# Kernel optimization log

Measured on AMD Instinct MI355X. Metric: run time of the kernel, lower is better.

## Reference

```python
import jax, jax.numpy as jnp
import numpy as np

L, D, FF, V, B, S, H, GS = 6, 1024, 4096, 32000, 2, 1024, 16, 128
DH = D // H


def setup_inputs() -> dict:
    key = jax.random.key(0)
    ks = jax.random.split(key, 32)

    def tern(k, shape):
        # ternary values in {-1, 0, 1}, stored as float32 (int8 buffer in torch)
        return jax.random.randint(k, shape, -1, 2).astype(jnp.float32)

    def sc(k, shape):
        # positive per-group scales (abs-mean init, clamped > 0)
        return jax.random.uniform(k, shape, jnp.float32, 0.01, 0.1)

    inp = {
        'input_ids': jax.random.randint(ks[0], (B, S), 0, V),
        'emb_t': tern(ks[1], (V, D)),
        'emb_s': sc(ks[2], (V * D // GS,)),
        'pos_emb': jax.random.normal(ks[3], (S, D), jnp.float32) * 0.02,
        'q_t': tern(ks[4], (L, D, D)), 'q_s': sc(ks[5], (L, D * D // GS)),
        'k_t': tern(ks[6], (L, D, D)), 'k_s': sc(ks[7], (L, D * D // GS)),
        'v_t': tern(ks[8], (L, D, D)), 'v_s': sc(ks[9], (L, D * D // GS)),
        'o_t': tern(ks[10], (L, D, D)), 'o_s': sc(ks[11], (L, D * D // GS)),
        'g_t': tern(ks[12], (L, FF, D)), 'g_s': sc(ks[13], (L, D * FF // GS)),
        'u_t': tern(ks[14], (L, FF, D)), 'u_s': sc(ks[15], (L, D * FF // GS)),
        'd_t': tern(ks[16], (L, D, FF)), 'd_s': sc(ks[17], (L, D * FF // GS)),
        'alpha': jnp.full((L, H, 1, 1), 0.1, jnp.float32),
        'na_w': jnp.ones((L, D), jnp.float32),
        'nm_w': jnp.ones((L, D), jnp.float32),
        'nf_w': jnp.ones((D,), jnp.float32),
        'head_t': tern(ks[18], (V, D)),
        'head_s': sc(ks[19], (V * D // GS,)),
    }
    return inp


def _dq(t, s):
    # dequantize: reshape ternary to (..., n_groups, GS), scale per group
    tg = t.reshape(t.shape[:-2] + (-1, GS))
    return (tg * s[..., :, None]).reshape(t.shape)


def _rms(x, w, eps=1e-6):
    return x * jax.lax.rsqrt(jnp.mean(x * x, axis=-1, keepdims=True) + eps) * w


def _forward(input_ids, emb_t, emb_s, pos_emb, q_t, q_s, k_t, k_s, v_t, v_s,
             o_t, o_s, g_t, g_s, u_t, u_s, d_t, d_s, alpha, na_w, nm_w, nf_w,
             head_t, head_s):
    x = _dq(emb_t, emb_s)[input_ids] + pos_emb[None, :S]  # [B,S,D]
    causal = jnp.tril(jnp.ones((S, S), bool))
    scale = DH ** -0.5

    def block(x, p):
        (qt, qs, kt, ks_, vt, vs, ot, os_, gt, gs_, ut, us, dt, ds,
         al, naw, nmw) = p
        h = _rms(x, naw)

        def proj(t, s):
            return (h @ _dq(t, s).T).reshape(B, S, H, DH).transpose(0, 2, 1, 3)

        q, k, v = proj(qt, qs), proj(kt, ks_), proj(vt, vs)
        att = jnp.einsum('bhqd,bhkd->bhqk', q, k) * scale
        att = jax.nn.softmax(jnp.where(causal, att, -jnp.inf), axis=-1)
        out = jnp.einsum('bhqk,bhkd->bhqd', att, v)
        # residual head-mix: out += alpha * x_heads (x here is the normed input h)
        out = out + al * h.reshape(B, S, H, DH).transpose(0, 2, 1, 3)
        out = out.transpose(0, 2, 1, 3).reshape(B, S, D)
        x = x + out @ _dq(ot, os_).T
        h2 = _rms(x, nmw)
        gate = h2 @ _dq(gt, gs_).T
        up = h2 @ _dq(ut, us).T
        x = x + (jax.nn.silu(gate) * up) @ _dq(dt, ds).T
        return x, None

    params = (q_t, q_s, k_t, k_s, v_t, v_s, o_t, o_s, g_t, g_s, u_t, u_s,
              d_t, d_s, alpha, na_w, nm_w)
    x, _ = jax.lax.scan(block, x, params)
    x = _rms(x, nf_w)
    return x @ _dq(head_t, head_s).T  # [B,S,V]


def reference(input_ids, emb_t, emb_s, pos_emb, q_t, q_s, k_t, k_s, v_t, v_s,
              o_t, o_s, g_t, g_s, u_t, u_s, d_t, d_s, alpha, na_w, nm_w, nf_w,
              head_t, head_s):
    return _forward(input_ids, emb_t, emb_s, pos_emb, q_t, q_s, k_t, k_s,
                    v_t, v_s, o_t, o_s, g_t, g_s, u_t, u_s, d_t, d_s,
                    alpha, na_w, nm_w, nf_w, head_t, head_s)
```

## Files before the change

### kernel.cpp

```cpp
#include <hip/hip_runtime.h>
#include <math.h>

#define Lc   6
#define Dc   1024
#define FFc  4096
#define Vc   32000
#define Bc   2
#define Sc   1024
#define Hc   16
#define GSc  128
#define DHc  64
#define Mc   (Bc * Sc)

typedef __attribute__((ext_vector_type(8))) short bf16x8;
typedef __attribute__((ext_vector_type(4))) float f32x4;

__device__ inline unsigned ph2(float a, float b) {
    return (__float_as_uint(b) & 0xffff0000u) | (__float_as_uint(a) >> 16);
}
__device__ inline float flo(float a) {
    return a - __uint_as_float(__float_as_uint(a) & 0xffff0000u);
}
__device__ inline ushort bhi(float a) { return (ushort)(__float_as_uint(a) >> 16); }
__device__ inline ushort blo(float a) { return (ushort)(__float_as_uint(flo(a)) >> 16); }
__device__ inline float unbf(ushort h) { return __uint_as_float((unsigned)h << 16); }

__device__ inline size_t swz_bidx(int row, int col, int K) {
    size_t byte = (size_t)col * 2;
    size_t base = (size_t)row * K * 2 + (byte & ~(size_t)127);
    int inner = (int)(byte & 127);
    inner = (inner & 15) | ((((inner >> 4) ^ (row & 7)) & 7) << 4);
    return base + (size_t)inner;
}

__device__ inline void glds16(const void* g, void* l) {
    __builtin_amdgcn_global_load_lds(
        (const __attribute__((address_space(1))) void*)g,
        (__attribute__((address_space(3))) void*)l, 16, 0, 0);
}

__device__ inline float block_reduce_sum(float v, float* scratch) {
    __syncthreads();
    int lane = threadIdx.x & 63, w = threadIdx.x >> 6;
#pragma unroll
    for (int off = 32; off > 0; off >>= 1) v += __shfl_down(v, off, 64);
    if (lane == 0) scratch[w] = v;
    __syncthreads();
    if (threadIdx.x == 0) scratch[0] = scratch[0] + scratch[1] + scratch[2] + scratch[3];
    __syncthreads();
    return scratch[0];
}

__global__ __launch_bounds__(256) void k_embed(const int* __restrict__ ids,
                                               const float* __restrict__ et,
                                               const float* __restrict__ es,
                                               const float* __restrict__ pos,
                                               float* __restrict__ x) {
    int row = blockIdx.x;
    int sp  = row & (Sc - 1);
    int d   = threadIdx.x << 2;
    int idx = ids[row];
    int base = idx * Dc + d;
    float4 t = *(const float4*)(et + base);
    float  s = es[base >> 7];
    float4 p = *(const float4*)(pos + sp * Dc + d);
    float4 o;
    o.x = fmaf(t.x, s, p.x); o.y = fmaf(t.y, s, p.y);
    o.z = fmaf(t.z, s, p.z); o.w = fmaf(t.w, s, p.w);
    *(float4*)(x + row * Dc + d) = o;
}

__global__ __launch_bounds__(256) void k_rmsnorm_bf(const float* __restrict__ x,
                                                    const float* __restrict__ w,
                                                    ushort* __restrict__ hi,
                                                    ushort* __restrict__ lo) {
    __shared__ float scratch[4];
    int row = blockIdx.x;
    int d = threadIdx.x << 2;
    float4 f = *(const float4*)(x + (size_t)row * Dc + d);
    float s = f.x * f.x + f.y * f.y + f.z * f.z + f.w * f.w;
    s = block_reduce_sum(s, scratch);
    float rinv = rsqrtf(s * (1.0f / Dc) + 1e-6f);
    float4 wv = *(const float4*)(w + d);
    float o0 = f.x * rinv * wv.x, o1 = f.y * rinv * wv.y;
    float o2 = f.z * rinv * wv.z, o3 = f.w * rinv * wv.w;
    ushort4 hv, lv;
    hv.x = bhi(o0); hv.y = bhi(o1); hv.z = bhi(o2); hv.w = bhi(o3);
    lv.x = blo(o0); lv.y = blo(o1); lv.z = blo(o2); lv.w = blo(o3);
    const size_t sb = swz_bidx(row, d, Dc);
    *(ushort4*)((char*)hi + sb) = hv;
    *(ushort4*)((char*)lo + sb) = lv;
}

template <bool RESID>
__device__ __forceinline__ void gemm_core(
    const ushort* __restrict__ Ahi, const ushort* __restrict__ Alo,
    const float* __restrict__ Wt, const float* __restrict__ Ws,
    const float* __restrict__ R, float* __restrict__ C,
    const int bn, const int N, const int K, const int g0, const int g1) {
    __shared__ char Ah[16384];
    __shared__ char Al[16384];
    __shared__ char Bh[16384];
    __shared__ float Wsl[128];

    const int tid  = threadIdx.x;
    const int lane = tid & 63;
    const int wv   = tid >> 6;
    const int wm   = (wv >> 1) << 6;
    const int wn   = (wv & 1) << 6;
    const int bm   = blockIdx.x << 7;
    const int kg   = K >> 7;

    const int sr   = tid >> 1;
    const int sh   = tid & 1;
    const int swr  = (sr & 7) << 4;
    const int rowb = sr << 7;
    const int colb = sh << 6;
    const float* Bbase = Wt + (size_t)(bn + sr) * K + (sh << 5);

    const int gr = (wv << 3) + (lane >> 3);
    const int gc = (lane & 7) << 4;
    const char* Abh = (const char*)Ahi;
    const char* Abl = (const char*)Alo;

    const int lr  = lane & 15;
    const int lkb = (lane >> 4) << 4;
    const int frs = (lane & 7) << 4;

    f32x4 acc[4][4], accg[4][4];
#pragma unroll
    for (int i = 0; i < 4; ++i)
#pragma unroll
        for (int j = 0; j < 4; ++j) {
            acc[i][j]  = (f32x4){0.f, 0.f, 0.f, 0.f};
            accg[i][j] = (f32x4){0.f, 0.f, 0.f, 0.f};
        }

    float4 bv[8];
    const int s0 = g0 << 1, s1 = g1 << 1;
    {
        const float4* p = (const float4*)(Bbase + (s0 << 6));
#pragma unroll
        for (int jj = 0; jj < 8; ++jj) bv[jj] = p[jj];
    }

    for (int s = s0; s < s1; ++s) {
        const int k0 = s << 6;
        __syncthreads();
#pragma unroll
        for (int i = 0; i < 4; ++i) {
            const size_t sb = ((size_t)(bm + gr + (i << 5)) * K + k0) * 2 + gc;
            glds16(Abh + sb, Ah + (wv << 10) + (i << 12));
            glds16(Abl + sb, Al + (wv << 10) + (i << 12));
        }
        if ((s & 1) == 0 && tid < 128)
            Wsl[tid] = Ws[(size_t)(bn + tid) * kg + (s >> 1)];
#pragma unroll
        for (int j = 0; j < 4; ++j) {
            const int ob = rowb + ((colb + (j << 4)) ^ swr);
            float4 x0 = bv[2 * j], x1 = bv[2 * j + 1];
            *(uint4*)(Bh + ob) = make_uint4(ph2(x0.x, x0.y), ph2(x0.z, x0.w),
                                            ph2(x1.x, x1.y), ph2(x1.z, x1.w));
        }
        __syncthreads();
        if (s + 1 < s1) {
            const float4* p = (const float4*)(Bbase + ((s + 1) << 6));
#pragma unroll
            for (int jj = 0; jj < 8; ++jj) bv[jj] = p[jj];
        }
#pragma unroll
        for (int ks = 0; ks < 2; ++ks) {
            bf16x8 fa[4], fl[4], fb[4];
            const int cb = ((ks << 6) + lkb) ^ frs;
#pragma unroll
            for (int f = 0; f < 4; ++f) {
                const int ra = (wm + (f << 4) + lr) << 7;
                fa[f] = *(const bf16x8*)(Ah + ra + cb);
                fl[f] = *(const bf16x8*)(Al + ra + cb);
                const int rb = (wn + (f << 4) + lr) << 7;
                fb[f] = *(const bf16x8*)(Bh + rb + cb);
            }
#pragma unroll
            for (int i = 0; i < 4; ++i)
#pragma unroll
                for (int j = 0; j < 4; ++j) {
                    accg[i][j] = __builtin_amdgcn_mfma_f32_16x16x32_bf16(fa[i], fb[j], accg[i][j], 0, 0, 0);
                    accg[i][j] = __builtin_amdgcn_mfma_f32_16x16x32_bf16(fl[i], fb[j], accg[i][j], 0, 0, 0);
                }
        }
        if (s & 1) {
            float sv[4];
#pragma unroll
            for (int j = 0; j < 4; ++j) sv[j] = Wsl[wn + (j << 4) + lr];
#pragma unroll
            for (int i = 0; i < 4; ++i)
#pragma unroll
                for (int j = 0; j < 4; ++j) {
                    acc[i][j] += accg[i][j] * sv[j];
                    accg[i][j] = (f32x4){0.f, 0.f, 0.f, 0.f};
                }
        }
    }

    const int r0 = bm + wm + ((lane >> 4) << 2);
    const int c0 = bn + wn + lr;
#pragma unroll
    for (int i = 0; i < 4; ++i) {
        const int row = r0 + (i << 4);
#pragma unroll
        for (int j = 0; j < 4; ++j) {
            size_t off = (size_t)row * N + c0 + (j << 4);
#pragma unroll
            for (int e = 0; e < 4; ++e) {
                float vv = acc[i][j][e];
                if (RESID) vv += R[off];
                C[off] = vv;
                off += (size_t)N;
            }
        }
    }
}

template <bool RESID>
__global__ __launch_bounds__(256, 2) void k_gemm_bfa(
    const ushort* __restrict__ Ahi, const ushort* __restrict__ Alo,
    const float* __restrict__ Wt, const float* __restrict__ Ws,
    const float* __restrict__ R, float* __restrict__ C, int N, int K) {
    gemm_core<RESID>(Ahi, Alo, Wt, Ws, R, C, blockIdx.y << 7, N, K, 0, K >> 7);
}

__global__ __launch_bounds__(256, 2) void k_gemm_part(
    const ushort* __restrict__ Ahi, const ushort* __restrict__ Alo,
    const float* __restrict__ Wt, const float* __restrict__ Ws,
    float* __restrict__ P, int N, int K, int gper) {
    const int z = blockIdx.z;
    gemm_core<false>(Ahi, Alo, Wt, Ws, nullptr, P + (size_t)z * Mc * Dc,
                     blockIdx.y << 7, N, K, z * gper, (z + 1) * gper);
}

__global__ __launch_bounds__(256, 2) void k_gemm_qkv(
    const ushort* __restrict__ Ahi, const ushort* __restrict__ Alo,
    const float* __restrict__ qt, const float* __restrict__ qs,
    const float* __restrict__ kt, const float* __restrict__ ks,
    const float* __restrict__ vt, const float* __restrict__ vs,
    float* __restrict__ qb, float* __restrict__ kb, float* __restrict__ vb) {
    const int which = blockIdx.y >> 3;
    const int bn = (blockIdx.y & 7) << 7;
    const float* Wt = which == 0 ? qt : which == 1 ? kt : vt;
    const float* Ws = which == 0 ? qs : which == 1 ? ks : vs;
    float* C = which == 0 ? qb : which == 1 ? kb : vb;
    gemm_core<false>(Ahi, Alo, Wt, Ws, nullptr, C, bn, Dc, Dc, 0, Dc >> 7);
}

__global__ __launch_bounds__(256, 2) void k_gemm_gu(
    const ushort* __restrict__ Ahi, const ushort* __restrict__ Alo,
    const float* __restrict__ gt, const float* __restrict__ gs,
    const float* __restrict__ ut, const float* __restrict__ us,
    float* __restrict__ gate, float* __restrict__ up) {
    const int which = blockIdx.y >> 5;
    const int bn = (blockIdx.y & 31) << 7;
    const float* Wt = which == 0 ? gt : ut;
    const float* Ws = which == 0 ? gs : us;
    float* C = which == 0 ? gate : up;
    gemm_core<false>(Ahi, Alo, Wt, Ws, nullptr, C, bn, FFc, Dc, 0, Dc >> 7);
}

__global__ __launch_bounds__(256) void k_red4(const float* __restrict__ p,
                                              float* __restrict__ x) {
    const size_t i = (((size_t)blockIdx.x << 8) + threadIdx.x) << 2;
    const size_t st = (size_t)Mc * Dc;
    float4 a  = *(const float4*)(x + i);
    float4 p0 = *(const float4*)(p + i);
    float4 p1 = *(const float4*)(p + i + st);
    float4 p2 = *(const float4*)(p + i + 2 * st);
    float4 p3 = *(const float4*)(p + i + 3 * st);
    a.x += p0.x + p1.x + p2.x + p3.x;
    a.y += p0.y + p1.y + p2.y + p3.y;
    a.z += p0.z + p1.z + p2.z + p3.z;
    a.w += p0.w + p1.w + p2.w + p3.w;
    *(float4*)(x + i) = a;
}

__global__ __launch_bounds__(256) void k_silumul(const float* __restrict__ g,
                                                 const float* __restrict__ u,
                                                 ushort* __restrict__ fhi,
                                                 ushort* __restrict__ fl2) {
    const size_t i = (((size_t)blockIdx.x << 8) + threadIdx.x) << 2;
    float4 gv = *(const float4*)(g + i);
    float4 uv = *(const float4*)(u + i);
    float r0 = uv.x * (gv.x / (1.0f + expf(-gv.x)));
    float r1 = uv.y * (gv.y / (1.0f + expf(-gv.y)));
    float r2 = uv.z * (gv.z / (1.0f + expf(-gv.z)));
    float r3 = uv.w * (gv.w / (1.0f + expf(-gv.w)));
    ushort4 hv, lv;
    hv.x = bhi(r0); hv.y = bhi(r1); hv.z = bhi(r2); hv.w = bhi(r3);
    lv.x = blo(r0); lv.y = blo(r1); lv.z = blo(r2); lv.w = blo(r3);
    const int row = (int)(i >> 12);
    const int col = (int)(i & 4095);
    const size_t sb = swz_bidx(row, col, FFc);
    *(ushort4*)((char*)fhi + sb) = hv;
    *(ushort4*)((char*)fl2 + sb) = lv;
}

__global__ __launch_bounds__(256, 2) void k_attn_mfma(
    const float* __restrict__ q, const float* __restrict__ k,
    const float* __restrict__ v, const ushort* __restrict__ hnhi,
    const ushort* __restrict__ hnlo, const float* __restrict__ alpha,
    ushort* __restrict__ aohi, ushort* __restrict__ aolo) {
    __shared__ uint4 KhV[512], KlV[512];
    __shared__ uint4 VthV[512], VtlV[512];
    __shared__ uint4 PhV[512], PlV[512];
    char* Khc  = (char*)KhV;
    char* Klc  = (char*)KlV;
    char* Vthc = (char*)VthV;
    char* Vtlc = (char*)VtlV;

    const int t = blockIdx.x, hh = blockIdx.y, b = blockIdx.z;
    const int tid  = threadIdx.x;
    const int lane = tid & 63, w = tid >> 6;
    const int lr = lane & 15, g = lane >> 4;
    const int bS = b * Sc;
    const int hoff = hh * DHc;

    char* myPh = (char*)PhV + (w << 11);
    char* myPl = (char*)PlV + (w << 11);

    const int qrow = (t << 6) + (w << 4) + lr;
    bf16x8 qh[2], ql[2];
    {
        const float* qp = q + (size_t)(bS + qrow) * Dc + hoff + (g << 3);
#pragma unroll
        for (int c = 0; c < 2; ++c) {
            float4 f0 = *(const float4*)(qp + (c << 5));
            float4 f1 = *(const float4*)(qp + (c << 5) + 4);
            float s[8] = {f0.x * 0.125f, f0.y * 0.125f, f0.z * 0.125f, f0.w * 0.125f,
                          f1.x * 0.125f, f1.y * 0.125f, f1.z * 0.125f, f1.w * 0.125f};
            union { bf16x8 v; unsigned u[4]; } Hh, Ll;
#pragma unroll
            for (int p = 0; p < 4; ++p) {
                Hh.u[p] = ph2(s[2 * p], s[2 * p + 1]);
                Ll.u[p] = ph2(flo(s[2 * p]), flo(s[2 * p + 1]));
            }
            qh[c] = Hh.v; ql[c] = Ll.v;
        }
    }

    f32x4 oacc[4];
    float m[4], lsum[4];
#pragma unroll
    for (int f = 0; f < 4; ++f) oacc[f] = (f32x4){0.f, 0.f, 0.f, 0.f};
#pragma unroll
    for (int e = 0; e < 4; ++e) { m[e] = -3.0e38f; lsum[e] = 0.f; }

    const int skey = tid >> 2, sseg = tid & 3;
    const int k4 = (tid >> 4) << 2, d4 = (tid & 15) << 2;

    float4 kr[4], vr[4];
    {
        const float* src = k + (size_t)(bS + skey) * Dc + hoff + (sseg << 4);
#pragma unroll
        for (int r = 0; r < 4; ++r) kr[r] = *(const float4*)(src + (r << 2));
        const float* vsrc = v + (size_t)(bS + k4) * Dc + hoff + d4;
#pragma unroll
        for (int r = 0; r < 4; ++r) vr[r] = *(const float4*)(vsrc + r * Dc);
    }

    const int nt = t + 1;
    for (int j = 0; j < nt; ++j) {
        {
            const int swz = (skey & 7) << 4;
            char* dsth = Khc + skey * 128;
            char* dstl = Klc + skey * 128;
            float4 a0 = kr[0], a1 = kr[1], a2 = kr[2], a3 = kr[3];
            *(uint4*)(dsth + (((sseg << 5)) ^ swz)) =
                make_uint4(ph2(a0.x, a0.y), ph2(a0.z, a0.w), ph2(a1.x, a1.y), ph2(a1.z, a1.w));
            *(uint4*)(dsth + (((sseg << 5) + 16) ^ swz)) =
                make_uint4(ph2(a2.x, a2.y), ph2(a2.z, a2.w), ph2(a3.x, a3.y), ph2(a3.z, a3.w));
            *(uint4*)(dstl + (((sseg << 5)) ^ swz)) =
                make_uint4(ph2(flo(a0.x), flo(a0.y)), ph2(flo(a0.z), flo(a0.w)),
                           ph2(flo(a1.x), flo(a1.y)), ph2(flo(a1.z), flo(a1.w)));
            *(uint4*)(dstl + (((sseg << 5) + 16) ^ swz)) =
                make_uint4(ph2(flo(a2.x), flo(a2.y)), ph2(flo(a2.z), flo(a2.w)),
                           ph2(flo(a3.x), flo(a3.y)), ph2(flo(a3.z), flo(a3.w)));
        }
        {
            union { float4 v4; float f[4]; } r0, r1, r2, r3;
            r0.v4 = vr[0]; r1.v4 = vr[1]; r2.v4 = vr[2]; r3.v4 = vr[3];
#pragma unroll
            for (int d = 0; d < 4; ++d) {
                const int dh = d4 + d;
                const int byt = dh * 128 + (((k4 << 1)) ^ ((dh & 7) << 4));
                float x0 = r0.f[d], x1 = r1.f[d], x2 = r2.f[d], x3 = r3.f[d];
                *(uint2*)(Vthc + byt) = make_uint2(ph2(x0, x1), ph2(x2, x3));
                *(uint2*)(Vtlc + byt) =
                    make_uint2(ph2(flo(x0), flo(x1)), ph2(flo(x2), flo(x3)));
            }
        }
        __syncthreads();
        if (j + 1 < nt) {
            const int kb2 = (j + 1) << 6;
            const float* src = k + (size_t)(bS + kb2 + skey) * Dc + hoff + (sseg << 4);
#pragma unroll
            for (int r = 0; r < 4; ++r) kr[r] = *(const float4*)(src + (r << 2));
            const float* vsrc = v + (size_t)(bS + kb2 + k4) * Dc + hoff + d4;
#pragma unroll
            for (int r = 0; r < 4; ++r) vr[r] = *(const float4*)(vsrc + r * Dc);
        }

        f32x4 sacc[4];
#pragma unroll
        for (int f = 0; f < 4; ++f) sacc[f] = (f32x4){0.f, 0.f, 0.f, 0.f};
#pragma unroll
        for (int c = 0; c < 2; ++c) {
            const int cb = (c << 6) + (g << 4);
#pragma unroll
            for (int f = 0; f < 4; ++f) {
                const int row = (f << 4) + lr;
                const int byt = row * 128 + (cb ^ ((row & 7) << 4));
                bf16x8 kh = *(const bf16x8*)(Khc + byt);
                bf16x8 kl = *(const bf16x8*)(Klc + byt);
                sacc[f] = __builtin_amdgcn_mfma_f32_16x16x32_bf16(qh[c], kh, sacc[f], 0, 0, 0);
                sacc[f] = __builtin_amdgcn_mfma_f32_16x16x32_bf16(ql[c], kh, sacc[f], 0, 0, 0);
                sacc[f] = __builtin_amdgcn_mfma_f32_16x16x32_bf16(qh[c], kl, sacc[f], 0, 0, 0);
            }
        }
        if (j == t) {
            const int qloc = (w << 4) + (g << 2);
#pragma unroll
            for (int f = 0; f < 4; ++f) {
                const int key = (f << 4) + lr;
#pragma unroll
                for (int e = 0; e < 4; ++e)
                    if (key > qloc + e) sacc[f][e] = -3.0e38f;
            }
        }
        float rmax[4], corr[4], rsum[4];
#pragma unroll
        for (int e = 0; e < 4; ++e)
            rmax[e] = fmaxf(fmaxf(sacc[0][e], sacc[1][e]), fmaxf(sacc[2][e], sacc[3][e]));
#pragma unroll
        for (int msk = 1; msk <= 8; msk <<= 1)
#pragma unroll
            for (int e = 0; e < 4; ++e)
                rmax[e] = fmaxf(rmax[e], __shfl_xor(rmax[e], msk, 64));
#pragma unroll
        for (int e = 0; e < 4; ++e) {
            float mn = fmaxf(m[e], rmax[e]);
            corr[e] = __expf(m[e] - mn);
            m[e] = mn;
            rsum[e] = 0.f;
        }
#pragma unroll
        for (int f = 0; f < 4; ++f)
#pragma unroll
            for (int e = 0; e < 4; ++e) {
                float p = __expf(sacc[f][e] - m[e]);
                sacc[f][e] = p;
                rsum[e] += p;
            }
#pragma unroll
        for (int msk = 1; msk <= 8; msk <<= 1)
#pragma unroll
            for (int e = 0; e < 4; ++e) rsum[e] += __shfl_xor(rsum[e], msk, 64);
#pragma unroll
        for (int e = 0; e < 4; ++e) lsum[e] = lsum[e] * corr[e] + rsum[e];
#pragma unroll
        for (int f = 0; f < 4; ++f)
#pragma unroll
            for (int e = 0; e < 4; ++e) oacc[f][e] *= corr[e];

#pragma unroll
        for (int f = 0; f < 4; ++f) {
            const int key2 = ((f << 4) + lr) << 1;
#pragma unroll
            for (int e = 0; e < 4; ++e) {
                const int qr = (g << 2) + e;
                const int byt = qr * 128 + (key2 ^ ((qr & 7) << 4));
                unsigned bits = __float_as_uint(sacc[f][e]);
                unsigned hib = bits & 0xffff0000u;
                *(short*)(myPh + byt) = (short)(hib >> 16);
                float lov = sacc[f][e] - __uint_as_float(hib);
                *(short*)(myPl + byt) = (short)(__float_as_uint(lov) >> 16);
            }
        }
#pragma unroll
        for (int c = 0; c < 2; ++c) {
            const int cb = (c << 6) + (g << 4);
            const int pbyt = lr * 128 + (cb ^ ((lr & 7) << 4));
            bf16x8 pah = *(const bf16x8*)(myPh + pbyt);
            bf16x8 pal = *(const bf16x8*)(myPl + pbyt);
#pragma unroll
            for (int f = 0; f < 4; ++f) {
                const int row = (f << 4) + lr;
                const int byt = row * 128 + (cb ^ ((row & 7) << 4));
                bf16x8 vbh = *(const bf16x8*)(Vthc + byt);
                bf16x8 vbl = *(const bf16x8*)(Vtlc + byt);
                oacc[f] = __builtin_amdgcn_mfma_f32_16x16x32_bf16(pah, vbh, oacc[f], 0, 0, 0);
                oacc[f] = __builtin_amdgcn_mfma_f32_16x16x32_bf16(pal, vbh, oacc[f], 0, 0, 0);
                oacc[f] = __builtin_amdgcn_mfma_f32_16x16x32_bf16(pah, vbl, oacc[f], 0, 0, 0);
            }
        }
        __syncthreads();
    }

    const float al = alpha[hh];
    float invl[4];
#pragma unroll
    for (int e = 0; e < 4; ++e) invl[e] = 1.0f / lsum[e];
#pragma unroll
    for (int f = 0; f < 4; ++f) {
        const int dh = (f << 4) + lr;
#pragma unroll
        for (int e = 0; e < 4; ++e) {
            const int qg = (t << 6) + (w << 4) + (g << 2) + e;
            const int row = bS + qg;
            const size_t sb = swz_bidx(row, hoff + dh, Dc);
            float hnv = unbf(*(const ushort*)((const char*)hnhi + sb)) +
                        unbf(*(const ushort*)((const char*)hnlo + sb));
            float val = fmaf(al, hnv, oacc[f][e] * invl[e]);
            *(ushort*)((char*)aohi + sb) = bhi(val);
            *(ushort*)((char*)aolo + sb) = blo(val);
        }
    }
}

extern "C" void kernel_launch(void* const* d_in, const int* in_sizes, int n_in,
                              void* d_out, int out_size, void* d_ws, size_t ws_size,
                              hipStream_t stream) {
    const int*   ids    = (const int*)d_in[0];
    const float* emb_t  = (const float*)d_in[1];
    const float* emb_s  = (const float*)d_in[2];
    const float* pos    = (const float*)d_in[3];
    const float* q_t    = (const float*)d_in[4];
    const float* q_s    = (const float*)d_in[5];
    const float* k_t    = (const float*)d_in[6];
    const float* k_s    = (const float*)d_in[7];
    const float* v_t    = (const float*)d_in[8];
    const float* v_s    = (const float*)d_in[9];
    const float* o_t    = (const float*)d_in[10];
    const float* o_s    = (const float*)d_in[11];
    const float* g_t    = (const float*)d_in[12];
    const float* g_s    = (const float*)d_in[13];
    const float* u_t    = (const float*)d_in[14];
    const float* u_s    = (const float*)d_in[15];
    const float* dd_t   = (const float*)d_in[16];
    const float* dd_s   = (const float*)d_in[17];
    const float* alpha  = (const float*)d_in[18];
    const float* na_w   = (const float*)d_in[19];
    const float* nm_w   = (const float*)d_in[20];
    const float* nf_w   = (const float*)d_in[21];
    const float* head_t = (const float*)d_in[22];
    const float* head_s = (const float*)d_in[23];
    float* outp = (float*)d_out;

    float*  ws   = (float*)d_ws;
    float*  x    = ws;
    ushort* hhi  = (ushort*)(x + (size_t)Mc * Dc);
    ushort* hlo  = hhi + (size_t)Mc * Dc;
    float*  big  = (float*)(hlo + (size_t)Mc * Dc);
    float*  qb   = big;
    float*  kb   = big + (size_t)Mc * Dc;
    float*  vb   = big + (size_t)2 * Mc * Dc;
    ushort* aohi = (ushort*)(big + (size_t)3 * Mc * Dc);
    ushort* aolo = aohi + (size_t)Mc * Dc;
    float*  up   = big;
    float*  gate = (float*)d_out;
    ushort* ffhi = (ushort*)((char*)d_out + (size_t)Mc * FFc * 4);
    ushort* fflo = ffhi + (size_t)Mc * FFc;

    k_embed<<<Mc, 256, 0, stream>>>(ids, emb_t, emb_s, pos, x);

    const dim3 gD(Mc / 128, Dc / 128);
    const dim3 gQKV(Mc / 128, 3 * Dc / 128);
    const dim3 gGU(Mc / 128, 2 * FFc / 128);
    const dim3 gDN(Mc / 128, Dc / 128, 4);
    const dim3 gH(Mc / 128, Vc / 128);
    const dim3 gA(Sc / 64, Hc, Bc);
    const int  gSilu = (Mc * FFc) / (256 * 4);
    const int  gRed  = (Mc * Dc) / (256 * 4);

    for (int l = 0; l < Lc; ++l) {
        const float* qt = q_t + (size_t)l * Dc * Dc;
        const float* qs = q_s + (size_t)l * (Dc * Dc / GSc);
        const float* kt = k_t + (size_t)l * Dc * Dc;
        const float* ks = k_s + (size_t)l * (Dc * Dc / GSc);
        const float* vt = v_t + (size_t)l * Dc * Dc;
        const float* vs = v_s + (size_t)l * (Dc * Dc / GSc);
        const float* ot = o_t + (size_t)l * Dc * Dc;
        const float* os = o_s + (size_t)l * (Dc * Dc / GSc);
        const float* gt = g_t + (size_t)l * FFc * Dc;
        const float* gs = g_s + (size_t)l * (FFc * Dc / GSc);
        const float* ut = u_t + (size_t)l * FFc * Dc;
        const float* us = u_s + (size_t)l * (FFc * Dc / GSc);
        const float* dt = dd_t + (size_t)l * Dc * FFc;
        const float* ds = dd_s + (size_t)l * (Dc * FFc / GSc);

        k_rmsnorm_bf<<<Mc, 256, 0, stream>>>(x, na_w + l * Dc, hhi, hlo);
        k_gemm_qkv<<<gQKV, 256, 0, stream>>>(hhi, hlo, qt, qs, kt, ks, vt, vs, qb, kb, vb);
        k_attn_mfma<<<gA, 256, 0, stream>>>(qb, kb, vb, hhi, hlo, alpha + l * Hc, aohi, aolo);
        k_gemm_bfa<true><<<gD, 256, 0, stream>>>(aohi, aolo, ot, os, x, x, Dc, Dc);
        k_rmsnorm_bf<<<Mc, 256, 0, stream>>>(x, nm_w + l * Dc, hhi, hlo);
        k_gemm_gu<<<gGU, 256, 0, stream>>>(hhi, hlo, gt, gs, ut, us, gate, up);
        k_silumul<<<gSilu, 256, 0, stream>>>(gate, up, ffhi, fflo);
        k_gemm_part<<<gDN, 256, 0, stream>>>(ffhi, fflo, dt, ds, big, Dc, FFc, 8);
        k_red4<<<gRed, 256, 0, stream>>>(big, x);
    }

    k_rmsnorm_bf<<<Mc, 256, 0, stream>>>(x, nf_w, hhi, hlo);
    k_gemm_bfa<false><<<gH, 256, 0, stream>>>(hhi, hlo, head_t, head_s, nullptr, outp, Vc, Dc);
}
```

Baseline: 3.144 ms.

## Pair causal attention tiles per block, split-K the O projection, raise GEMM occupancy

The attention kernel now gives each block two query tiles, t and its mirror from the end, so every block does the same amount of causal work and the grid is halved. The output projection moves from a residual-fused GEMM to a 4-way split-K partial GEMM followed by a reduction kernel, which adds more blocks for a small N=1024 GEMM. Launch bounds on the GEMM kernels go from 2 to 3 waves per SIMD, which may cause register spills. The split-K path adds an extra reduction pass and writes the partial sums through d_out as scratch.

```diff
diff --git a/kernel.cpp b/kernel.cpp
--- a/kernel.cpp
+++ b/kernel.cpp
@@ -38,6 +38,7 @@
         (const __attribute__((address_space(1))) void*)g,
         (__attribute__((address_space(3))) void*)l, 16, 0, 0);
 }
+
 
 __device__ inline float block_reduce_sum(float v, float* scratch) {
     __syncthreads();
@@ -202,7 +203,7 @@
         }
     }
 
-    const int r0 = bm + wm + ((lane >> 4) << 2);
+    const int r0 = (blockIdx.x << 7) + wm + ((lane >> 4) << 2);
     const int c0 = bn + wn + lr;
 #pragma unroll
     for (int i = 0; i < 4; ++i) {
@@ -221,15 +222,14 @@
     }
 }
 
-template <bool RESID>
-__global__ __launch_bounds__(256, 2) void k_gemm_bfa(
+__global__ __launch_bounds__(256, 3) void k_gemm_head(
     const ushort* __restrict__ Ahi, const ushort* __restrict__ Alo,
     const float* __restrict__ Wt, const float* __restrict__ Ws,
-    const float* __restrict__ R, float* __restrict__ C, int N, int K) {
-    gemm_core<RESID>(Ahi, Alo, Wt, Ws, R, C, blockIdx.y << 7, N, K, 0, K >> 7);
-}
-
-__global__ __launch_bounds__(256, 2) void k_gemm_part(
+    float* __restrict__ C, int N, int K) {
+    gemm_core<false>(Ahi, Alo, Wt, Ws, nullptr, C, blockIdx.y << 7, N, K, 0, K >> 7);
+}
+
+__global__ __launch_bounds__(256, 3) void k_gemm_part(
     const ushort* __restrict__ Ahi, const ushort* __restrict__ Alo,
     const float* __restrict__ Wt, const float* __restrict__ Ws,
     float* __restrict__ P, int N, int K, int gper) {
@@ -238,7 +238,7 @@
                      blockIdx.y << 7, N, K, z * gper, (z + 1) * gper);
 }
 
-__global__ __launch_bounds__(256, 2) void k_gemm_qkv(
+__global__ __launch_bounds__(256, 3) void k_gemm_qkv(
     const ushort* __restrict__ Ahi, const ushort* __restrict__ Alo,
     const float* __restrict__ qt, const float* __restrict__ qs,
     const float* __restrict__ kt, const float* __restrict__ ks,
@@ -252,7 +252,7 @@
     gemm_core<false>(Ahi, Alo, Wt, Ws, nullptr, C, bn, Dc, Dc, 0, Dc >> 7);
 }
 
-__global__ __launch_bounds__(256, 2) void k_gemm_gu(
+__global__ __launch_bounds__(256, 3) void k_gemm_gu(
     const ushort* __restrict__ Ahi, const ushort* __restrict__ Alo,
     const float* __restrict__ gt, const float* __restrict__ gs,
     const float* __restrict__ ut, const float* __restrict__ us,
@@ -315,212 +315,218 @@
     char* Vthc = (char*)VthV;
     char* Vtlc = (char*)VtlV;
 
-    const int t = blockIdx.x, hh = blockIdx.y, b = blockIdx.z;
+    const int hh = blockIdx.y, b = blockIdx.z;
     const int tid  = threadIdx.x;
     const int lane = tid & 63, w = tid >> 6;
     const int lr = lane & 15, g = lane >> 4;
     const int bS = b * Sc;
     const int hoff = hh * DHc;
+    const float al = alpha[hh];
 
     char* myPh = (char*)PhV + (w << 11);
     char* myPl = (char*)PlV + (w << 11);
 
-    const int qrow = (t << 6) + (w << 4) + lr;
-    bf16x8 qh[2], ql[2];
-    {
-        const float* qp = q + (size_t)(bS + qrow) * Dc + hoff + (g << 3);
-#pragma unroll
-        for (int c = 0; c < 2; ++c) {
-            float4 f0 = *(const float4*)(qp + (c << 5));
-            float4 f1 = *(const float4*)(qp + (c << 5) + 4);
-            float s[8] = {f0.x * 0.125f, f0.y * 0.125f, f0.z * 0.125f, f0.w * 0.125f,
-                          f1.x * 0.125f, f1.y * 0.125f, f1.z * 0.125f, f1.w * 0.125f};
-            union { bf16x8 v; unsigned u[4]; } Hh, Ll;
-#pragma unroll
-            for (int p = 0; p < 4; ++p) {
-                Hh.u[p] = ph2(s[2 * p], s[2 * p + 1]);
-                Ll.u[p] = ph2(flo(s[2 * p]), flo(s[2 * p + 1]));
-            }
-            qh[c] = Hh.v; ql[c] = Ll.v;
-        }
-    }
-
-    f32x4 oacc[4];
-    float m[4], lsum[4];
-#pragma unroll
-    for (int f = 0; f < 4; ++f) oacc[f] = (f32x4){0.f, 0.f, 0.f, 0.f};
-#pragma unroll
-    for (int e = 0; e < 4; ++e) { m[e] = -3.0e38f; lsum[e] = 0.f; }
-
     const int skey = tid >> 2, sseg = tid & 3;
     const int k4 = (tid >> 4) << 2, d4 = (tid & 15) << 2;
 
-    float4 kr[4], vr[4];
-    {
-        const float* src = k + (size_t)(bS + skey) * Dc + hoff + (sseg << 4);
-#pragma unroll
-        for (int r = 0; r < 4; ++r) kr[r] = *(const float4*)(src + (r << 2));
-        const float* vsrc = v + (size_t)(bS + k4) * Dc + hoff + d4;
-#pragma unroll
-        for (int r = 0; r < 4; ++r) vr[r] = *(const float4*)(vsrc + r * Dc);
-    }
-
-    const int nt = t + 1;
-    for (int j = 0; j < nt; ++j) {
+#pragma unroll 1
+    for (int half = 0; half < 2; ++half) {
+        const int t = half ? ((Sc / 64) - 1 - (int)blockIdx.x) : (int)blockIdx.x;
+
+        const int qrow = (t << 6) + (w << 4) + lr;
+        bf16x8 qh[2], ql[2];
         {
-            const int swz = (skey & 7) << 4;
-            char* dsth = Khc + skey * 128;
-            char* dstl = Klc + skey * 128;
-            float4 a0 = kr[0], a1 = kr[1], a2 = kr[2], a3 = kr[3];
-            *(uint4*)(dsth + (((sseg << 5)) ^ swz)) =
-                make_uint4(ph2(a0.x, a0.y), ph2(a0.z, a0.w), ph2(a1.x, a1.y), ph2(a1.z, a1.w));
-            *(uint4*)(dsth + (((sseg << 5) + 16) ^ swz)) =
-                make_uint4(ph2(a2.x, a2.y), ph2(a2.z, a2.w), ph2(a3.x, a3.y), ph2(a3.z, a3.w));
-            *(uint4*)(dstl + (((sseg << 5)) ^ swz)) =
-                make_uint4(ph2(flo(a0.x), flo(a0.y)), ph2(flo(a0.z), flo(a0.w)),
-                           ph2(flo(a1.x), flo(a1.y)), ph2(flo(a1.z), flo(a1.w)));
-            *(uint4*)(dstl + (((sseg << 5) + 16) ^ swz)) =
-                make_uint4(ph2(flo(a2.x), flo(a2.y)), ph2(flo(a2.z), flo(a2.w)),
-                           ph2(flo(a3.x), flo(a3.y)), ph2(flo(a3.z), flo(a3.w)));
-        }
+            const float* qp = q + (size_t)(bS + qrow) * Dc + hoff + (g << 3);
+#pragma unroll
+            for (int c = 0; c < 2; ++c) {
+                float4 f0 = *(const float4*)(qp + (c << 5));
+                float4 f1 = *(const float4*)(qp + (c << 5) + 4);
+                float s[8] = {f0.x * 0.125f, f0.y * 0.125f, f0.z * 0.125f, f0.w * 0.125f,
+                              f1.x * 0.125f, f1.y * 0.125f, f1.z * 0.125f, f1.w * 0.125f};
+                union { bf16x8 v; unsigned u[4]; } Hh, Ll;
+#pragma unroll
+                for (int p = 0; p < 4; ++p) {
+                    Hh.u[p] = ph2(s[2 * p], s[2 * p + 1]);
+                    Ll.u[p] = ph2(flo(s[2 * p]), flo(s[2 * p + 1]));
+                }
+                qh[c] = Hh.v; ql[c] = Ll.v;
+            }
+        }
+
+        f32x4 oacc[4];
+        float m[4], lsum[4];
+#pragma unroll
+        for (int f = 0; f < 4; ++f) oacc[f] = (f32x4){0.f, 0.f, 0.f, 0.f};
+#pragma unroll
+        for (int e = 0; e < 4; ++e) { m[e] = -3.0e38f; lsum[e] = 0.f; }
+
+        float4 kr[4], vr[4];
         {
-            union { float4 v4; float f[4]; } r0, r1, r2, r3;
-            r0.v4 = vr[0]; r1.v4 = vr[1]; r2.v4 = vr[2]; r3.v4 = vr[3];
-#pragma unroll
-            for (int d = 0; d < 4; ++d) {
-                const int dh = d4 + d;
-                const int byt = dh * 128 + (((k4 << 1)) ^ ((dh & 7) << 4));
-                float x0 = r0.f[d], x1 = r1.f[d], x2 = r2.f[d], x3 = r3.f[d];
-                *(uint2*)(Vthc + byt) = make_uint2(ph2(x0, x1), ph2(x2, x3));
-                *(uint2*)(Vtlc + byt) =
-                    make_uint2(ph2(flo(x0), flo(x1)), ph2(flo(x2), flo(x3)));
+            const float* src = k + (size_t)(bS + skey) * Dc + hoff + (sseg << 4);
+#pragma unroll
+            for (int r = 0; r < 4; ++r) kr[r] = *(const float4*)(src + (r << 2));
+            const float* vsrc = v + (size_t)(bS + k4) * Dc + hoff + d4;
+#pragma unroll
+            for (int r = 0; r < 4; ++r) vr[r] = *(const float4*)(vsrc + r * Dc);
+        }
+
+        const int nt = t + 1;
+        for (int j = 0; j < nt; ++j) {
+            {
+                const int swz = (skey & 7) << 4;
+                char* dsth = Khc + skey * 128;
+                char* dstl = Klc + skey * 128;
+                float4 a0 = kr[0], a1 = kr[1], a2 = kr[2], a3 = kr[3];
+                *(uint4*)(dsth + (((sseg << 5)) ^ swz)) =
+                    make_uint4(ph2(a0.x, a0.y), ph2(a0.z, a0.w), ph2(a1.x, a1.y), ph2(a1.z, a1.w));
+                *(uint4*)(dsth + (((sseg << 5) + 16) ^ swz)) =
+                    make_uint4(ph2(a2.x, a2.y), ph2(a2.z, a2.w), ph2(a3.x, a3.y), ph2(a3.z, a3.w));
+                *(uint4*)(dstl + (((sseg << 5)) ^ swz)) =
+                    make_uint4(ph2(flo(a0.x), flo(a0.y)), ph2(flo(a0.z), flo(a0.w)),
+                               ph2(flo(a1.x), flo(a1.y)), ph2(flo(a1.z), flo(a1.w)));
+                *(uint4*)(dstl + (((sseg << 5) + 16) ^ swz)) =
+                    make_uint4(ph2(flo(a2.x), flo(a2.y)), ph2(flo(a2.z), flo(a2.w)),
+                               ph2(flo(a3.x), flo(a3.y)), ph2(flo(a3.z), flo(a3.w)));
+            }
+            {
+                union { float4 v4; float f[4]; } r0, r1, r2, r3;
+                r0.v4 = vr[0]; r1.v4 = vr[1]; r2.v4 = vr[2]; r3.v4 = vr[3];
+#pragma unroll
+                for (int d = 0; d < 4; ++d) {
+                    const int dh = d4 + d;
+                    const int byt = dh * 128 + (((k4 << 1)) ^ ((dh & 7) << 4));
+                    float x0 = r0.f[d], x1 = r1.f[d], x2 = r2.f[d], x3 = r3.f[d];
+                    *(uint2*)(Vthc + byt) = make_uint2(ph2(x0, x1), ph2(x2, x3));
+                    *(uint2*)(Vtlc + byt) =
+                        make_uint2(ph2(flo(x0), flo(x1)), ph2(flo(x2), flo(x3)));
+                }
+            }
+            __syncthreads();
+            if (j + 1 < nt) {
+                const int kb2 = (j + 1) << 6;
+                const float* src = k + (size_t)(bS + kb2 + skey) * Dc + hoff + (sseg << 4);
+#pragma unroll
+                for (int r = 0; r < 4; ++r) kr[r] = *(const float4*)(src + (r << 2));
+                const float* vsrc = v + (size_t)(bS + kb2 + k4) * Dc + hoff + d4;
+#pragma unroll
+                for (int r = 0; r < 4; ++r) vr[r] = *(const float4*)(vsrc + r * Dc);
+            }
+
+            f32x4 sacc[4];
+#pragma unroll
+            for (int f = 0; f < 4; ++f) sacc[f] = (f32x4){0.f, 0.f, 0.f, 0.f};
+#pragma unroll
+            for (int c = 0; c < 2; ++c) {
+                const int cb = (c << 6) + (g << 4);
+#pragma unroll
+                for (int f = 0; f < 4; ++f) {
+                    const int row = (f << 4) + lr;
+                    const int byt = row * 128 + (cb ^ ((row & 7) << 4));
+                    bf16x8 kh = *(const bf16x8*)(Khc + byt);
+                    bf16x8 kl = *(const bf16x8*)(Klc + byt);
+                    sacc[f] = __builtin_amdgcn_mfma_f32_16x16x32_bf16(qh[c], kh, sacc[f], 0, 0, 0);
+                    sacc[f] = __builtin_amdgcn_mfma_f32_16x16x32_bf16(ql[c], kh, sacc[f], 0, 0, 0);
+                    sacc[f] = __builtin_amdgcn_mfma_f32_16x16x32_bf16(qh[c], kl, sacc[f], 0, 0, 0);
+                }
+            }
+            if (j == t) {
+                const int qloc = (w << 4) + (g << 2);
+#pragma unroll
+                for (int f = 0; f < 4; ++f) {
+                    const int key = (f << 4) + lr;
+#pragma unroll
+                    for (int e = 0; e < 4; ++e)
+                        if (key > qloc + e) sacc[f][e] = -3.0e38f;
+                }
+            }
+            float rmax[4], corr[4], rsum[4];
+#pragma unroll
+            for (int e = 0; e < 4; ++e)
+                rmax[e] = fmaxf(fmaxf(sacc[0][e], sacc[1][e]), fmaxf(sacc[2][e], sacc[3][e]));
+#pragma unroll
+            for (int msk = 1; msk <= 8; msk <<= 1)
+#pragma unroll
+                for (int e = 0; e < 4; ++e)
+                    rmax[e] = fmaxf(rmax[e], __shfl_xor(rmax[e], msk, 64));
+#pragma unroll
+            for (int e = 0; e < 4; ++e) {
+                float mn = fmaxf(m[e], rmax[e]);
+                corr[e] = __expf(m[e] - mn);
+                m[e] = mn;
+                rsum[e] = 0.f;
+            }
+#pragma unroll
+            for (int f = 0; f < 4; ++f)
+#pragma unroll
+                for (int e = 0; e < 4; ++e) {
+                    float p = __expf(sacc[f][e] - m[e]);
+                    sacc[f][e] = p;
+                    rsum[e] += p;
+                }
+#pragma unroll
+            for (int msk = 1; msk <= 8; msk <<= 1)
+#pragma unroll
+                for (int e = 0; e < 4; ++e) rsum[e] += __shfl_xor(rsum[e], msk, 64);
+#pragma unroll
+            for (int e = 0; e < 4; ++e) lsum[e] = lsum[e] * corr[e] + rsum[e];
+#pragma unroll
+            for (int f = 0; f < 4; ++f)
+#pragma unroll
+                for (int e = 0; e < 4; ++e) oacc[f][e] *= corr[e];
+
+#pragma unroll
+            for (int f = 0; f < 4; ++f) {
+                const int key2 = ((f << 4) + lr) << 1;
+#pragma unroll
+                for (int e = 0; e < 4; ++e) {
+                    const int qr = (g << 2) + e;
+                    const int byt = qr * 128 + (key2 ^ ((qr & 7) << 4));
+                    unsigned bits = __float_as_uint(sacc[f][e]);
+                    unsigned hib = bits & 0xffff0000u;
+                    *(short*)(myPh + byt) = (short)(hib >> 16);
+                    float lov = sacc[f][e] - __uint_as_float(hib);
+                    *(short*)(myPl + byt) = (short)(__float_as_uint(lov) >> 16);
+                }
+            }
+#pragma unroll
+            for (int c = 0; c < 2; ++c) {
+                const int cb = (c << 6) + (g << 4);
+                const int pbyt = lr * 128 + (cb ^ ((lr & 7) << 4));
+                bf16x8 pah = *(const bf16x8*)(myPh + pbyt);
+                bf16x8 pal = *(const bf16x8*)(myPl + pbyt);
+#pragma unroll
+                for (int f = 0; f < 4; ++f) {
+                    const int row = (f << 4) + lr;
+                    const int byt = row * 128 + (cb ^ ((row & 7) << 4));
+                    bf16x8 vbh = *(const bf16x8*)(Vthc + byt);
+                    bf16x8 vbl = *(const bf16x8*)(Vtlc + byt);
+                    oacc[f] = __builtin_amdgcn_mfma_f32_16x16x32_bf16(pah, vbh, oacc[f], 0, 0, 0);
+                    oacc[f] = __builtin_amdgcn_mfma_f32_16x16x32_bf16(pal, vbh, oacc[f], 0, 0, 0);
+                    oacc[f] = __builtin_amdgcn_mfma_f32_16x16x32_bf16(pah, vbl, oacc[f], 0, 0, 0);
+                }
+            }
+            __syncthreads();
+        }
+
+        float invl[4];
+#pragma unroll
+        for (int e = 0; e < 4; ++e) invl[e] = 1.0f / lsum[e];
+#pragma unroll
+        for (int f = 0; f < 4; ++f) {
+            const int dh = (f << 4) + lr;
+#pragma unroll
+            for (int e = 0; e < 4; ++e) {
+                const int qg = (t << 6) + (w << 4) + (g << 2) + e;
+                const int row = bS + qg;
+                const size_t sb = swz_bidx(row, hoff + dh, Dc);
+                float hnv = unbf(*(const ushort*)((const char*)hnhi + sb)) +
+                            unbf(*(const ushort*)((const char*)hnlo + sb));
+                float val = fmaf(al, hnv, oacc[f][e] * invl[e]);
+                *(ushort*)((char*)aohi + sb) = bhi(val);
+                *(ushort*)((char*)aolo + sb) = blo(val);
             }
         }
         __syncthreads();
-        if (j + 1 < nt) {
-            const int kb2 = (j + 1) << 6;
-            const float* src = k + (size_t)(bS + kb2 + skey) * Dc + hoff + (sseg << 4);
-#pragma unroll
-            for (int r = 0; r < 4; ++r) kr[r] = *(const float4*)(src + (r << 2));
-            const float* vsrc = v + (size_t)(bS + kb2 + k4) * Dc + hoff + d4;
-#pragma unroll
-            for (int r = 0; r < 4; ++r) vr[r] = *(const float4*)(vsrc + r * Dc);
-        }
-
-        f32x4 sacc[4];
-#pragma unroll
-        for (int f = 0; f < 4; ++f) sacc[f] = (f32x4){0.f, 0.f, 0.f, 0.f};
-#pragma unroll
-        for (int c = 0; c < 2; ++c) {
-            const int cb = (c << 6) + (g << 4);
-#pragma unroll
-            for (int f = 0; f < 4; ++f) {
-                const int row = (f << 4) + lr;
-                const int byt = row * 128 + (cb ^ ((row & 7) << 4));
-                bf16x8 kh = *(const bf16x8*)(Khc + byt);
-                bf16x8 kl = *(const bf16x8*)(Klc + byt);
-                sacc[f] = __builtin_amdgcn_mfma_f32_16x16x32_bf16(qh[c], kh, sacc[f], 0, 0, 0);
-                sacc[f] = __builtin_amdgcn_mfma_f32_16x16x32_bf16(ql[c], kh, sacc[f], 0, 0, 0);
-                sacc[f] = __builtin_amdgcn_mfma_f32_16x16x32_bf16(qh[c], kl, sacc[f], 0, 0, 0);
-            }
-        }
-        if (j == t) {
-            const int qloc = (w << 4) + (g << 2);
-#pragma unroll
-            for (int f = 0; f < 4; ++f) {
-                const int key = (f << 4) + lr;
-#pragma unroll
-                for (int e = 0; e < 4; ++e)
-                    if (key > qloc + e) sacc[f][e] = -3.0e38f;
-            }
-        }
-        float rmax[4], corr[4], rsum[4];
-#pragma unroll
-        for (int e = 0; e < 4; ++e)
-            rmax[e] = fmaxf(fmaxf(sacc[0][e], sacc[1][e]), fmaxf(sacc[2][e], sacc[3][e]));
-#pragma unroll
-        for (int msk = 1; msk <= 8; msk <<= 1)
-#pragma unroll
-            for (int e = 0; e < 4; ++e)
-                rmax[e] = fmaxf(rmax[e], __shfl_xor(rmax[e], msk, 64));
-#pragma unroll
-        for (int e = 0; e < 4; ++e) {
-            float mn = fmaxf(m[e], rmax[e]);
-            corr[e] = __expf(m[e] - mn);
-            m[e] = mn;
-            rsum[e] = 0.f;
-        }
-#pragma unroll
-        for (int f = 0; f < 4; ++f)
-#pragma unroll
-            for (int e = 0; e < 4; ++e) {
-                float p = __expf(sacc[f][e] - m[e]);
-                sacc[f][e] = p;
-                rsum[e] += p;
-            }
-#pragma unroll
-        for (int msk = 1; msk <= 8; msk <<= 1)
-#pragma unroll
-            for (int e = 0; e < 4; ++e) rsum[e] += __shfl_xor(rsum[e], msk, 64);
-#pragma unroll
-        for (int e = 0; e < 4; ++e) lsum[e] = lsum[e] * corr[e] + rsum[e];
-#pragma unroll
-        for (int f = 0; f < 4; ++f)
-#pragma unroll
-            for (int e = 0; e < 4; ++e) oacc[f][e] *= corr[e];
-
-#pragma unroll
-        for (int f = 0; f < 4; ++f) {
-            const int key2 = ((f << 4) + lr) << 1;
-#pragma unroll
-            for (int e = 0; e < 4; ++e) {
-                const int qr = (g << 2) + e;
-                const int byt = qr * 128 + (key2 ^ ((qr & 7) << 4));
-                unsigned bits = __float_as_uint(sacc[f][e]);
-                unsigned hib = bits & 0xffff0000u;
-                *(short*)(myPh + byt) = (short)(hib >> 16);
-                float lov = sacc[f][e] - __uint_as_float(hib);
-                *(short*)(myPl + byt) = (short)(__float_as_uint(lov) >> 16);
-            }
-        }
-#pragma unroll
-        for (int c = 0; c < 2; ++c) {
-            const int cb = (c << 6) + (g << 4);
-            const int pbyt = lr * 128 + (cb ^ ((lr & 7) << 4));
-            bf16x8 pah = *(const bf16x8*)(myPh + pbyt);
-            bf16x8 pal = *(const bf16x8*)(myPl + pbyt);
-#pragma unroll
-            for (int f = 0; f < 4; ++f) {
-                const int row = (f << 4) + lr;
-                const int byt = row * 128 + (cb ^ ((row & 7) << 4));
-                bf16x8 vbh = *(const bf16x8*)(Vthc + byt);
-                bf16x8 vbl = *(const bf16x8*)(Vtlc + byt);
-                oacc[f] = __builtin_amdgcn_mfma_f32_16x16x32_bf16(pah, vbh, oacc[f], 0, 0, 0);
-                oacc[f] = __builtin_amdgcn_mfma_f32_16x16x32_bf16(pal, vbh, oacc[f], 0, 0, 0);
-                oacc[f] = __builtin_amdgcn_mfma_f32_16x16x32_bf16(pah, vbl, oacc[f], 0, 0, 0);
-            }
-        }
-        __syncthreads();
-    }
-
-    const float al = alpha[hh];
-    float invl[4];
-#pragma unroll
-    for (int e = 0; e < 4; ++e) invl[e] = 1.0f / lsum[e];
-#pragma unroll
-    for (int f = 0; f < 4; ++f) {
-        const int dh = (f << 4) + lr;
-#pragma unroll
-        for (int e = 0; e < 4; ++e) {
-            const int qg = (t << 6) + (w << 4) + (g << 2) + e;
-            const int row = bS + qg;
-            const size_t sb = swz_bidx(row, hoff + dh, Dc);
-            float hnv = unbf(*(const ushort*)((const char*)hnhi + sb)) +
-                        unbf(*(const ushort*)((const char*)hnlo + sb));
-            float val = fmaf(al, hnv, oacc[f][e] * invl[e]);
-            *(ushort*)((char*)aohi + sb) = bhi(val);
-            *(ushort*)((char*)aolo + sb) = blo(val);
-        }
     }
 }
 
@@ -565,17 +571,17 @@
     ushort* aolo = aohi + (size_t)Mc * Dc;
     float*  up   = big;
     float*  gate = (float*)d_out;
+    float*  partO = (float*)d_out;
     ushort* ffhi = (ushort*)((char*)d_out + (size_t)Mc * FFc * 4);
     ushort* fflo = ffhi + (size_t)Mc * FFc;
 
     k_embed<<<Mc, 256, 0, stream>>>(ids, emb_t, emb_s, pos, x);
 
-    const dim3 gD(Mc / 128, Dc / 128);
-    const dim3 gQKV(Mc / 128, 3 * Dc / 128);
-    const dim3 gGU(Mc / 128, 2 * FFc / 128);
-    const dim3 gDN(Mc / 128, Dc / 128, 4);
+    const dim3 gQKV(Mc / 128, 24);
+    const dim3 gGU(Mc / 128, 64);
+    const dim3 gSK(Mc / 128, 8, 4);
     const dim3 gH(Mc / 128, Vc / 128);
-    const dim3 gA(Sc / 64, Hc, Bc);
+    const dim3 gA(Sc / 128, Hc, Bc);
     const int  gSilu = (Mc * FFc) / (256 * 4);
     const int  gRed  = (Mc * Dc) / (256 * 4);
 
@@ -598,14 +604,15 @@
         k_rmsnorm_bf<<<Mc, 256, 0, stream>>>(x, na_w + l * Dc, hhi, hlo);
         k_gemm_qkv<<<gQKV, 256, 0, stream>>>(hhi, hlo, qt, qs, kt, ks, vt, vs, qb, kb, vb);
         k_attn_mfma<<<gA, 256, 0, stream>>>(qb, kb, vb, hhi, hlo, alpha + l * Hc, aohi, aolo);
-        k_gemm_bfa<true><<<gD, 256, 0, stream>>>(aohi, aolo, ot, os, x, x, Dc, Dc);
+        k_gemm_part<<<gSK, 256, 0, stream>>>(aohi, aolo, ot, os, partO, Dc, Dc, 2);
+        k_red4<<<gRed, 256, 0, stream>>>(partO, x);
         k_rmsnorm_bf<<<Mc, 256, 0, stream>>>(x, nm_w + l * Dc, hhi, hlo);
         k_gemm_gu<<<gGU, 256, 0, stream>>>(hhi, hlo, gt, gs, ut, us, gate, up);
         k_silumul<<<gSilu, 256, 0, stream>>>(gate, up, ffhi, fflo);
-        k_gemm_part<<<gDN, 256, 0, stream>>>(ffhi, fflo, dt, ds, big, Dc, FFc, 8);
+        k_gemm_part<<<gSK, 256, 0, stream>>>(ffhi, fflo, dt, ds, big, Dc, FFc, 8);
         k_red4<<<gRed, 256, 0, stream>>>(big, x);
     }
 
     k_rmsnorm_bf<<<Mc, 256, 0, stream>>>(x, nf_w, hhi, hlo);
-    k_gemm_bfa<false><<<gH, 256, 0, stream>>>(hhi, hlo, head_t, head_s, nullptr, outp, Vc, Dc);
-}
+    k_gemm_head<<<gH, 256, 0, stream>>>(hhi, hlo, head_t, head_s, outp, Vc, Dc);
+}
```

After: 5.142 ms. 63.6% more time.
